# Optimization experiments

Hardware: AMD Instinct MI355X
Metric: run time of the kernel (lower is better)

The kernel has to match this reference:

```python
import jax, jax.numpy as jnp
import numpy as np

NUM_HEADS = 8

def setup_inputs() -> dict:
    key = jax.random.key(0)
    ks = jax.random.split(key, 6)
    B, nW, F_W, ED = 8, 64, 128, 512
    x = jax.random.normal(ks[0], (B * nW, F_W, ED), dtype=jnp.float32)
    adj_mask = jax.random.normal(ks[1], (B, NUM_HEADS, F_W, F_W), dtype=jnp.float32)
    qkv_w = jax.random.normal(ks[2], (ED, 3 * ED), dtype=jnp.float32) * (ED ** -0.5)
    qkv_b = jax.random.normal(ks[3], (3 * ED,), dtype=jnp.float32) * 0.02
    proj_w = jax.random.normal(ks[4], (ED, ED), dtype=jnp.float32) * (ED ** -0.5)
    proj_b = jax.random.normal(ks[5], (ED,), dtype=jnp.float32) * 0.02
    return {"x": x, "adj_mask": adj_mask, "qkv_w": qkv_w, "qkv_b": qkv_b,
            "proj_w": proj_w, "proj_b": proj_b, "B": B, "nW": nW}

def reference(x, adj_mask, qkv_w, qkv_b, proj_w, proj_b, B, nW):
    B_nW, F_W, ED = x.shape
    H = NUM_HEADS
    hd = ED // H
    scale = hd ** -0.5
    # qkv projection: [B_nW, F_W, 3, H, hd]
    qkv = (x @ qkv_w + qkv_b).reshape(B_nW, F_W, 3, H, hd)
    qkv = jnp.transpose(qkv, (2, 0, 3, 1, 4))  # [3, B_nW, H, F_W, hd]
    q, k, v = qkv[0], qkv[1], qkv[2]
    attn = jnp.einsum('bhqd,bhkd->bhqk', q * scale, k)  # [B_nW, H, F_W, F_W]
    # additive adjacency mask, broadcast over windows
    attn = attn.reshape(B, nW, H, F_W, F_W) + adj_mask[:, None]
    attn = attn.reshape(B_nW, H, F_W, F_W)
    attn = jax.nn.softmax(attn, axis=-1)
    out = jnp.einsum('bhqk,bhkd->bhqd', attn, v)  # [B_nW, H, F_W, hd]
    out = jnp.transpose(out, (0, 2, 1, 3)).reshape(B_nW, F_W, ED)
    return out @ proj_w + proj_b
```

## Files before the change

### kernel.cpp

```cpp
#include <hip/hip_runtime.h>

typedef __bf16 bf16_t;
typedef __bf16 bf16x4 __attribute__((ext_vector_type(4)));
typedef __bf16 bf16x8 __attribute__((ext_vector_type(8)));
typedef float f32x4 __attribute__((ext_vector_type(4)));

#define MFMA16(a, b, c) __builtin_amdgcn_mfma_f32_16x16x32_bf16(a, b, c, 0, 0, 0)

#define F_W 128
#define ED 512
#define NH 8
#define HD 64
#define B_NW 512

#define XS_STRIDE 40
#define WTS_STRIDE 40
#define QK_STRIDE 72
#define VT_STRIDE 136
#define P_STRIDE 136

__global__ __launch_bounds__(256) void prep_kernel(
    const float* __restrict__ qkv_w,
    const float* __restrict__ proj_w,
    bf16_t* __restrict__ qkv_wt,
    bf16_t* __restrict__ proj_wt) {
    int idx = blockIdx.x * 256 + threadIdx.x;
    if (idx < 1536 * 512) {
        int n = idx >> 9, k = idx & 511;
        qkv_wt[idx] = (bf16_t)qkv_w[k * 1536 + n];
    }
    if (idx < 512 * 512) {
        int n = idx >> 9, k = idx & 511;
        proj_wt[idx] = (bf16_t)proj_w[k * 512 + n];
    }
}

__global__ __launch_bounds__(256) void fused_attn_kernel(
    const float* __restrict__ x,
    const float* __restrict__ adj,
    const float* __restrict__ qkv_b,
    const bf16_t* __restrict__ qkv_wt,
    bf16_t* __restrict__ attn_out) {
    __shared__ bf16_t smem[27136];
    bf16_t* x_s  = smem;
    bf16_t* wt_s = smem + 5120;
    bf16_t* q_lds = smem;
    bf16_t* k_lds = smem + 9216;
    bf16_t* p_lds = smem;
    bf16_t* vt_lds = smem + 18432;

    const int tid  = threadIdx.x;
    const int wave = tid >> 6;
    const int lane = tid & 63;
    const int lrow = lane & 15;
    const int lgrp = lane >> 4;
    const int w = blockIdx.x >> 3;
    const int h = blockIdx.x & 7;
    const int bidx = w >> 6;

    const float* xw = x + (size_t)w * F_W * ED;

    f32x4 acc[2][12];
#pragma unroll
    for (int mf = 0; mf < 2; ++mf)
#pragma unroll
        for (int nf = 0; nf < 12; ++nf) acc[mf][nf] = (f32x4)0.0f;

    for (int kc = 0; kc < 16; ++kc) {
        const int k0 = kc * 32;
        __syncthreads();
#pragma unroll
        for (int i = 0; i < 4; ++i) {
            int linear = tid + i * 256;
            int row = linear >> 3, f4 = linear & 7;
            const float4 v = *(const float4*)(xw + (size_t)row * ED + k0 + f4 * 4);
            bf16x4 bv = {(bf16_t)v.x, (bf16_t)v.y, (bf16_t)v.z, (bf16_t)v.w};
            *(bf16x4*)(x_s + row * XS_STRIDE + f4 * 4) = bv;
        }
#pragma unroll
        for (int i = 0; i < 3; ++i) {
            int linear = tid + i * 256;
            int row = linear >> 2, seg = linear & 3;
            int ng = (row >> 6) * 512 + h * 64 + (row & 63);
            bf16x8 v = *(const bf16x8*)(qkv_wt + (size_t)ng * 512 + k0 + seg * 8);
            *(bf16x8*)(wt_s + row * WTS_STRIDE + seg * 8) = v;
        }
        __syncthreads();
        bf16x8 a[2], b[12];
#pragma unroll
        for (int mf = 0; mf < 2; ++mf)
            a[mf] = *(const bf16x8*)(x_s + (wave * 32 + mf * 16 + lrow) * XS_STRIDE + lgrp * 8);
#pragma unroll
        for (int nf = 0; nf < 12; ++nf)
            b[nf] = *(const bf16x8*)(wt_s + (nf * 16 + lrow) * WTS_STRIDE + lgrp * 8);
#pragma unroll
        for (int mf = 0; mf < 2; ++mf)
#pragma unroll
            for (int nf = 0; nf < 12; ++nf)
                acc[mf][nf] = MFMA16(a[mf], b[nf], acc[mf][nf]);
    }
    __syncthreads();

#pragma unroll
    for (int mf = 0; mf < 2; ++mf) {
#pragma unroll
        for (int nf = 0; nf < 12; ++nf) {
            int s = nf >> 2;
            int dl = (nf & 3) * 16 + lrow;
            float bias = qkv_b[s * 512 + h * 64 + dl];
#pragma unroll
            for (int j = 0; j < 4; ++j) {
                int row = wave * 32 + mf * 16 + lgrp * 4 + j;
                float val = acc[mf][nf][j] + bias;
                if (s == 0)      q_lds[row * QK_STRIDE + dl] = (bf16_t)(val * 0.125f);
                else if (s == 1) k_lds[row * QK_STRIDE + dl] = (bf16_t)val;
                else             vt_lds[dl * VT_STRIDE + row] = (bf16_t)val;
            }
        }
    }
    __syncthreads();

    f32x4 sacc[2][8];
#pragma unroll
    for (int mf = 0; mf < 2; ++mf)
#pragma unroll
        for (int nf = 0; nf < 8; ++nf) sacc[mf][nf] = (f32x4)0.0f;

#pragma unroll
    for (int kb = 0; kb < 2; ++kb) {
        bf16x8 a[2], b[8];
#pragma unroll
        for (int mf = 0; mf < 2; ++mf)
            a[mf] = *(const bf16x8*)(q_lds + (wave * 32 + mf * 16 + lrow) * QK_STRIDE + kb * 32 + lgrp * 8);
#pragma unroll
        for (int nf = 0; nf < 8; ++nf)
            b[nf] = *(const bf16x8*)(k_lds + (nf * 16 + lrow) * QK_STRIDE + kb * 32 + lgrp * 8);
#pragma unroll
        for (int mf = 0; mf < 2; ++mf)
#pragma unroll
            for (int nf = 0; nf < 8; ++nf)
                sacc[mf][nf] = MFMA16(a[mf], b[nf], sacc[mf][nf]);
    }

    const float* mbase = adj + ((size_t)(bidx * NH + h)) * F_W * F_W;
#pragma unroll
    for (int mf = 0; mf < 2; ++mf) {
#pragma unroll
        for (int j = 0; j < 4; ++j) {
            int row = wave * 32 + mf * 16 + lgrp * 4 + j;
            const float* mrow = mbase + (size_t)row * F_W;
            float mx = -1e30f;
#pragma unroll
            for (int nf = 0; nf < 8; ++nf) {
                sacc[mf][nf][j] += mrow[nf * 16 + lrow];
                mx = fmaxf(mx, sacc[mf][nf][j]);
            }
#pragma unroll
            for (int d = 1; d < 16; d <<= 1) mx = fmaxf(mx, __shfl_xor(mx, d));
            float sum = 0.f;
#pragma unroll
            for (int nf = 0; nf < 8; ++nf) {
                float p = exp2f((sacc[mf][nf][j] - mx) * 1.44269504f);
                sacc[mf][nf][j] = p;
                sum += p;
            }
#pragma unroll
            for (int d = 1; d < 16; d <<= 1) sum += __shfl_xor(sum, d);
            float r = 1.0f / sum;
#pragma unroll
            for (int nf = 0; nf < 8; ++nf) sacc[mf][nf][j] *= r;
        }
    }
    __syncthreads();
#pragma unroll
    for (int mf = 0; mf < 2; ++mf)
#pragma unroll
        for (int nf = 0; nf < 8; ++nf)
#pragma unroll
            for (int j = 0; j < 4; ++j) {
                int row = wave * 32 + mf * 16 + lgrp * 4 + j;
                p_lds[row * P_STRIDE + nf * 16 + lrow] = (bf16_t)sacc[mf][nf][j];
            }
    __syncthreads();

    f32x4 oacc[2][4];
#pragma unroll
    for (int mf = 0; mf < 2; ++mf)
#pragma unroll
        for (int nf = 0; nf < 4; ++nf) oacc[mf][nf] = (f32x4)0.0f;

#pragma unroll
    for (int kb = 0; kb < 4; ++kb) {
        bf16x8 a[2], b[4];
#pragma unroll
        for (int mf = 0; mf < 2; ++mf)
            a[mf] = *(const bf16x8*)(p_lds + (wave * 32 + mf * 16 + lrow) * P_STRIDE + kb * 32 + lgrp * 8);
#pragma unroll
        for (int nf = 0; nf < 4; ++nf)
            b[nf] = *(const bf16x8*)(vt_lds + (nf * 16 + lrow) * VT_STRIDE + kb * 32 + lgrp * 8);
#pragma unroll
        for (int mf = 0; mf < 2; ++mf)
#pragma unroll
            for (int nf = 0; nf < 4; ++nf)
                oacc[mf][nf] = MFMA16(a[mf], b[nf], oacc[mf][nf]);
    }

    bf16_t* obase = attn_out + (size_t)w * F_W * ED + h * HD;
#pragma unroll
    for (int mf = 0; mf < 2; ++mf)
#pragma unroll
        for (int nf = 0; nf < 4; ++nf)
#pragma unroll
            for (int j = 0; j < 4; ++j) {
                int row = wave * 32 + mf * 16 + lgrp * 4 + j;
                obase[(size_t)row * ED + nf * 16 + lrow] = (bf16_t)oacc[mf][nf][j];
            }
}

__global__ __launch_bounds__(256) void proj_kernel(
    const bf16_t* __restrict__ a_g,
    const bf16_t* __restrict__ bt_g,
    const float* __restrict__ bias,
    float* __restrict__ out) {
    __shared__ bf16_t a_s[128 * XS_STRIDE];
    __shared__ bf16_t b_s[128 * XS_STRIDE];
    const int tid = threadIdx.x;
    const int wave = tid >> 6, lane = tid & 63;
    const int lrow = lane & 15, lgrp = lane >> 4;
    const int mtile = blockIdx.x >> 2, ntile = blockIdx.x & 3;
    const size_t m0 = (size_t)mtile * 128;
    const int n0 = ntile * 128;

    f32x4 acc[2][8];
#pragma unroll
    for (int mf = 0; mf < 2; ++mf)
#pragma unroll
        for (int nf = 0; nf < 8; ++nf) acc[mf][nf] = (f32x4)0.0f;

    for (int kc = 0; kc < 16; ++kc) {
        const int k0 = kc * 32;
        __syncthreads();
#pragma unroll
        for (int i = 0; i < 2; ++i) {
            int linear = tid + i * 256;
            int row = linear >> 2, seg = linear & 3;
            *(bf16x8*)(a_s + row * XS_STRIDE + seg * 8) =
                *(const bf16x8*)(a_g + (m0 + row) * 512 + k0 + seg * 8);
            *(bf16x8*)(b_s + row * XS_STRIDE + seg * 8) =
                *(const bf16x8*)(bt_g + (size_t)(n0 + row) * 512 + k0 + seg * 8);
        }
        __syncthreads();
        bf16x8 a[2], b[8];
#pragma unroll
        for (int mf = 0; mf < 2; ++mf)
            a[mf] = *(const bf16x8*)(a_s + (wave * 32 + mf * 16 + lrow) * XS_STRIDE + lgrp * 8);
#pragma unroll
        for (int nf = 0; nf < 8; ++nf)
            b[nf] = *(const bf16x8*)(b_s + (nf * 16 + lrow) * XS_STRIDE + lgrp * 8);
#pragma unroll
        for (int mf = 0; mf < 2; ++mf)
#pragma unroll
            for (int nf = 0; nf < 8; ++nf)
                acc[mf][nf] = MFMA16(a[mf], b[nf], acc[mf][nf]);
    }

#pragma unroll
    for (int nf = 0; nf < 8; ++nf) {
        int col = n0 + nf * 16 + lrow;
        float bv = bias[col];
#pragma unroll
        for (int mf = 0; mf < 2; ++mf)
#pragma unroll
            for (int j = 0; j < 4; ++j) {
                size_t row = m0 + wave * 32 + mf * 16 + lgrp * 4 + j;
                out[row * 512 + col] = acc[mf][nf][j] + bv;
            }
    }
}

extern "C" void kernel_launch(void* const* d_in, const int* in_sizes, int n_in,
                              void* d_out, int out_size, void* d_ws, size_t ws_size,
                              hipStream_t stream) {
    const float* x      = (const float*)d_in[0];
    const float* adj    = (const float*)d_in[1];
    const float* qkv_w  = (const float*)d_in[2];
    const float* qkv_b  = (const float*)d_in[3];
    const float* proj_w = (const float*)d_in[4];
    const float* proj_b = (const float*)d_in[5];
    float* out = (float*)d_out;

    bf16_t* attn_out = (bf16_t*)d_ws;
    bf16_t* qkv_wt   = attn_out + (size_t)B_NW * F_W * ED;
    bf16_t* proj_wt  = qkv_wt + 1536 * 512;

    prep_kernel<<<3072, 256, 0, stream>>>(qkv_w, proj_w, qkv_wt, proj_wt);
    fused_attn_kernel<<<B_NW * NH, 256, 0, stream>>>(x, adj, qkv_b, qkv_wt, attn_out);
    proj_kernel<<<(B_NW * F_W / 128) * (ED / 128), 256, 0, stream>>>(attn_out, proj_wt, proj_b, out);
}
```

Baseline: 350.3 us.

## Use direct global-to-LDS loads with XOR-swizzled shared layouts in attention and proj

```diff
diff --git a/kernel.cpp b/kernel.cpp
--- a/kernel.cpp
+++ b/kernel.cpp
@@ -1,7 +1,6 @@
 #include <hip/hip_runtime.h>
 
 typedef __bf16 bf16_t;
-typedef __bf16 bf16x4 __attribute__((ext_vector_type(4)));
 typedef __bf16 bf16x8 __attribute__((ext_vector_type(8)));
 typedef float f32x4 __attribute__((ext_vector_type(4)));
 
@@ -13,11 +12,11 @@
 #define HD 64
 #define B_NW 512
 
-#define XS_STRIDE 40
-#define WTS_STRIDE 40
-#define QK_STRIDE 72
-#define VT_STRIDE 136
-#define P_STRIDE 136
+typedef const __attribute__((address_space(1))) void gvoid_t;
+typedef __attribute__((address_space(3))) void lvoid_t;
+__device__ __forceinline__ void gload16(const void* g, void* l) {
+    __builtin_amdgcn_global_load_lds((gvoid_t*)g, (lvoid_t*)l, 16, 0, 0);
+}
 
 __global__ __launch_bounds__(256) void prep_kernel(
     const float* __restrict__ qkv_w,
@@ -35,19 +34,19 @@
     }
 }
 
-__global__ __launch_bounds__(256) void fused_attn_kernel(
+__global__ __launch_bounds__(256, 3) void fused_attn_kernel(
     const float* __restrict__ x,
     const float* __restrict__ adj,
     const float* __restrict__ qkv_b,
     const bf16_t* __restrict__ qkv_wt,
     bf16_t* __restrict__ attn_out) {
-    __shared__ bf16_t smem[27136];
-    bf16_t* x_s  = smem;
-    bf16_t* wt_s = smem + 5120;
-    bf16_t* q_lds = smem;
-    bf16_t* k_lds = smem + 9216;
-    bf16_t* p_lds = smem;
-    bf16_t* vt_lds = smem + 18432;
+    __shared__ __align__(16) char smem[49152];
+    float*  x_s32  = (float*)smem;
+    bf16_t* wt_s   = (bf16_t*)(smem + 16384);
+    bf16_t* q_lds  = (bf16_t*)smem;
+    bf16_t* k_lds  = (bf16_t*)(smem + 16384);
+    bf16_t* p_lds  = (bf16_t*)smem;
+    bf16_t* vt_lds = (bf16_t*)(smem + 32768);
 
     const int tid  = threadIdx.x;
     const int wave = tid >> 6;
@@ -60,6 +59,11 @@
 
     const float* xw = x + (size_t)w * F_W * ED;
 
+    const int xrow_l = lane >> 3;
+    const int xcol_l = (((lane & 7) * 4) ^ ((xrow_l & 7) << 2));
+    const int wrow_l = lane >> 2;
+    const int wcol_l = ((((lane & 3) * 8)) ^ ((wrow_l & 3) << 3));
+
     f32x4 acc[2][12];
 #pragma unroll
     for (int mf = 0; mf < 2; ++mf)
@@ -71,28 +75,36 @@
         __syncthreads();
 #pragma unroll
         for (int i = 0; i < 4; ++i) {
-            int linear = tid + i * 256;
-            int row = linear >> 3, f4 = linear & 7;
-            const float4 v = *(const float4*)(xw + (size_t)row * ED + k0 + f4 * 4);
-            bf16x4 bv = {(bf16_t)v.x, (bf16_t)v.y, (bf16_t)v.z, (bf16_t)v.w};
-            *(bf16x4*)(x_s + row * XS_STRIDE + f4 * 4) = bv;
+            int c = wave * 4 + i;
+            const float* g = xw + (size_t)(c * 8 + xrow_l) * ED + k0 + xcol_l;
+            gload16(g, x_s32 + c * 256);
         }
 #pragma unroll
         for (int i = 0; i < 3; ++i) {
-            int linear = tid + i * 256;
-            int row = linear >> 2, seg = linear & 3;
-            int ng = (row >> 6) * 512 + h * 64 + (row & 63);
-            bf16x8 v = *(const bf16x8*)(qkv_wt + (size_t)ng * 512 + k0 + seg * 8);
-            *(bf16x8*)(wt_s + row * WTS_STRIDE + seg * 8) = v;
+            int c = wave * 3 + i;
+            int r = c * 16 + wrow_l;
+            int n = (r >> 6) * 512 + h * 64 + (r & 63);
+            const bf16_t* g = qkv_wt + (size_t)n * 512 + k0 + wcol_l;
+            gload16(g, wt_s + c * 512);
         }
         __syncthreads();
+
         bf16x8 a[2], b[12];
 #pragma unroll
-        for (int mf = 0; mf < 2; ++mf)
-            a[mf] = *(const bf16x8*)(x_s + (wave * 32 + mf * 16 + lrow) * XS_STRIDE + lgrp * 8);
-#pragma unroll
-        for (int nf = 0; nf < 12; ++nf)
-            b[nf] = *(const bf16x8*)(wt_s + (nf * 16 + lrow) * WTS_STRIDE + lgrp * 8);
+        for (int mf = 0; mf < 2; ++mf) {
+            int row = wave * 32 + mf * 16 + lrow;
+            int sw = (row & 7) << 2;
+            const float* px = x_s32 + row * 32;
+            f32x4 lo = *(const f32x4*)(px + ((lgrp * 8) ^ sw));
+            f32x4 hi = *(const f32x4*)(px + ((lgrp * 8 + 4) ^ sw));
+            a[mf] = bf16x8{(bf16_t)lo[0], (bf16_t)lo[1], (bf16_t)lo[2], (bf16_t)lo[3],
+                           (bf16_t)hi[0], (bf16_t)hi[1], (bf16_t)hi[2], (bf16_t)hi[3]};
+        }
+#pragma unroll
+        for (int nf = 0; nf < 12; ++nf) {
+            int row = nf * 16 + lrow;
+            b[nf] = *(const bf16x8*)(wt_s + row * 32 + ((lgrp * 8) ^ ((row & 3) << 3)));
+        }
 #pragma unroll
         for (int mf = 0; mf < 2; ++mf)
 #pragma unroll
@@ -112,9 +124,9 @@
             for (int j = 0; j < 4; ++j) {
                 int row = wave * 32 + mf * 16 + lgrp * 4 + j;
                 float val = acc[mf][nf][j] + bias;
-                if (s == 0)      q_lds[row * QK_STRIDE + dl] = (bf16_t)(val * 0.125f);
-                else if (s == 1) k_lds[row * QK_STRIDE + dl] = (bf16_t)val;
-                else             vt_lds[dl * VT_STRIDE + row] = (bf16_t)val;
+                if (s == 0)      q_lds[row * 64 + (dl ^ ((row & 7) << 3))] = (bf16_t)(val * 0.125f);
+                else if (s == 1) k_lds[row * 64 + (dl ^ ((row & 7) << 3))] = (bf16_t)val;
+                else             vt_lds[dl * 128 + (row ^ ((dl & 15) << 3))] = (bf16_t)val;
             }
         }
     }
@@ -130,11 +142,15 @@
     for (int kb = 0; kb < 2; ++kb) {
         bf16x8 a[2], b[8];
 #pragma unroll
-        for (int mf = 0; mf < 2; ++mf)
-            a[mf] = *(const bf16x8*)(q_lds + (wave * 32 + mf * 16 + lrow) * QK_STRIDE + kb * 32 + lgrp * 8);
-#pragma unroll
-        for (int nf = 0; nf < 8; ++nf)
-            b[nf] = *(const bf16x8*)(k_lds + (nf * 16 + lrow) * QK_STRIDE + kb * 32 + lgrp * 8);
+        for (int mf = 0; mf < 2; ++mf) {
+            int row = wave * 32 + mf * 16 + lrow;
+            a[mf] = *(const bf16x8*)(q_lds + row * 64 + ((kb * 32 + lgrp * 8) ^ ((row & 7) << 3)));
+        }
+#pragma unroll
+        for (int nf = 0; nf < 8; ++nf) {
+            int row = nf * 16 + lrow;
+            b[nf] = *(const bf16x8*)(k_lds + row * 64 + ((kb * 32 + lgrp * 8) ^ ((row & 7) << 3)));
+        }
 #pragma unroll
         for (int mf = 0; mf < 2; ++mf)
 #pragma unroll
@@ -149,10 +165,13 @@
         for (int j = 0; j < 4; ++j) {
             int row = wave * 32 + mf * 16 + lgrp * 4 + j;
             const float* mrow = mbase + (size_t)row * F_W;
+            float mval[8];
+#pragma unroll
+            for (int nf = 0; nf < 8; ++nf) mval[nf] = mrow[nf * 16 + lrow];
             float mx = -1e30f;
 #pragma unroll
             for (int nf = 0; nf < 8; ++nf) {
-                sacc[mf][nf][j] += mrow[nf * 16 + lrow];
+                sacc[mf][nf][j] += mval[nf];
                 mx = fmaxf(mx, sacc[mf][nf][j]);
             }
 #pragma unroll
@@ -179,7 +198,8 @@
 #pragma unroll
             for (int j = 0; j < 4; ++j) {
                 int row = wave * 32 + mf * 16 + lgrp * 4 + j;
-                p_lds[row * P_STRIDE + nf * 16 + lrow] = (bf16_t)sacc[mf][nf][j];
+                int col = nf * 16 + lrow;
+                p_lds[row * 128 + (col ^ ((row & 15) << 3))] = (bf16_t)sacc[mf][nf][j];
             }
     __syncthreads();
 
@@ -193,11 +213,15 @@
     for (int kb = 0; kb < 4; ++kb) {
         bf16x8 a[2], b[4];
 #pragma unroll
-        for (int mf = 0; mf < 2; ++mf)
-            a[mf] = *(const bf16x8*)(p_lds + (wave * 32 + mf * 16 + lrow) * P_STRIDE + kb * 32 + lgrp * 8);
-#pragma unroll
-        for (int nf = 0; nf < 4; ++nf)
-            b[nf] = *(const bf16x8*)(vt_lds + (nf * 16 + lrow) * VT_STRIDE + kb * 32 + lgrp * 8);
+        for (int mf = 0; mf < 2; ++mf) {
+            int row = wave * 32 + mf * 16 + lrow;
+            a[mf] = *(const bf16x8*)(p_lds + row * 128 + ((kb * 32 + lgrp * 8) ^ ((row & 15) << 3)));
+        }
+#pragma unroll
+        for (int nf = 0; nf < 4; ++nf) {
+            int d = nf * 16 + lrow;
+            b[nf] = *(const bf16x8*)(vt_lds + d * 128 + ((kb * 32 + lgrp * 8) ^ ((d & 15) << 3)));
+        }
 #pragma unroll
         for (int mf = 0; mf < 2; ++mf)
 #pragma unroll
@@ -222,14 +246,17 @@
     const bf16_t* __restrict__ bt_g,
     const float* __restrict__ bias,
     float* __restrict__ out) {
-    __shared__ bf16_t a_s[128 * XS_STRIDE];
-    __shared__ bf16_t b_s[128 * XS_STRIDE];
+    __shared__ __align__(16) bf16_t sm[8192];
+    bf16_t* a_s = sm;
+    bf16_t* b_s = sm + 4096;
     const int tid = threadIdx.x;
     const int wave = tid >> 6, lane = tid & 63;
     const int lrow = lane & 15, lgrp = lane >> 4;
     const int mtile = blockIdx.x >> 2, ntile = blockIdx.x & 3;
     const size_t m0 = (size_t)mtile * 128;
     const int n0 = ntile * 128;
+    const int wrow_l = lane >> 2;
+    const int wcol_l = ((((lane & 3) * 8)) ^ ((wrow_l & 3) << 3));
 
     f32x4 acc[2][8];
 #pragma unroll
@@ -242,21 +269,22 @@
         __syncthreads();
 #pragma unroll
         for (int i = 0; i < 2; ++i) {
-            int linear = tid + i * 256;
-            int row = linear >> 2, seg = linear & 3;
-            *(bf16x8*)(a_s + row * XS_STRIDE + seg * 8) =
-                *(const bf16x8*)(a_g + (m0 + row) * 512 + k0 + seg * 8);
-            *(bf16x8*)(b_s + row * XS_STRIDE + seg * 8) =
-                *(const bf16x8*)(bt_g + (size_t)(n0 + row) * 512 + k0 + seg * 8);
+            int c = wave * 2 + i;
+            gload16(a_g + (m0 + c * 16 + wrow_l) * 512 + k0 + wcol_l, a_s + c * 512);
+            gload16(bt_g + (size_t)(n0 + c * 16 + wrow_l) * 512 + k0 + wcol_l, b_s + c * 512);
         }
         __syncthreads();
         bf16x8 a[2], b[8];
 #pragma unroll
-        for (int mf = 0; mf < 2; ++mf)
-            a[mf] = *(const bf16x8*)(a_s + (wave * 32 + mf * 16 + lrow) * XS_STRIDE + lgrp * 8);
-#pragma unroll
-        for (int nf = 0; nf < 8; ++nf)
-            b[nf] = *(const bf16x8*)(b_s + (nf * 16 + lrow) * XS_STRIDE + lgrp * 8);
+        for (int mf = 0; mf < 2; ++mf) {
+            int row = wave * 32 + mf * 16 + lrow;
+            a[mf] = *(const bf16x8*)(a_s + row * 32 + ((lgrp * 8) ^ ((row & 3) << 3)));
+        }
+#pragma unroll
+        for (int nf = 0; nf < 8; ++nf) {
+            int row = nf * 16 + lrow;
+            b[nf] = *(const bf16x8*)(b_s + row * 32 + ((lgrp * 8) ^ ((row & 3) << 3)));
+        }
 #pragma unroll
         for (int mf = 0; mf < 2; ++mf)
 #pragma unroll
```

Measured after the change: 362.1 us. 1.03x slower.
